# Performance work log

Measured on AMD Instinct MI355X. Metric: run time of the kernel, lower is better.

## Reference

```python
import jax, jax.numpy as jnp
import numpy as np

DIM = 1024
NUM_EXPERTS = 8
ACTIVE_EXPERTS = 2
EXPERT_DIM = 2048


def setup_inputs() -> dict:
    key = jax.random.key(0)
    k1, k2, k3, k4 = jax.random.split(key, 4)
    x = jax.random.normal(k1, (1, 2048, DIM), dtype=jnp.float32)
    gate_w = jax.random.normal(k2, (NUM_EXPERTS, DIM), dtype=jnp.float32) * 0.02
    balance_bias = jnp.zeros((NUM_EXPERTS,), dtype=jnp.float32)
    w1 = jax.random.normal(k3, (NUM_EXPERTS, EXPERT_DIM, DIM), dtype=jnp.float32) * 0.02
    w2 = jax.random.normal(k4, (NUM_EXPERTS, DIM, EXPERT_DIM), dtype=jnp.float32) * 0.02
    return {"x": x, "gate_w": gate_w, "balance_bias": balance_bias, "w1": w1, "w2": w2}


def reference(x, gate_w, balance_bias, w1, w2):
    B, S, D = x.shape
    T = B * S
    xf = x.reshape(T, D)
    # gating: sigmoid scores with load-balance bias, then top-k
    gate_logits = jnp.einsum('td,ed->te', xf, gate_w)
    gate_scores = jax.nn.sigmoid(gate_logits + balance_bias)
    topk_scores, topk_idx = jax.lax.top_k(gate_scores, ACTIVE_EXPERTS)
    topk_scores = topk_scores / (topk_scores.sum(axis=-1, keepdims=True) + 1e-6)
    # scatter normalized scores into dense combine weights [T, E]
    comb = jnp.zeros((T, NUM_EXPERTS), dtype=x.dtype)
    comb = comb.at[jnp.arange(T)[:, None], topk_idx].add(topk_scores)
    # expert FFNs (dense over experts; combine weight zeroes unselected)
    h = jax.nn.silu(jnp.einsum('td,ehd->teh', xf, w1))   # [T, E, expert_dim]
    expert_out = jnp.einsum('teh,edh->ted', h, w2)        # [T, E, D]
    out = jnp.einsum('te,ted->td', comb, expert_out)
    return out.reshape(B, S, D)
```

## Files before the change

kernel.cpp:

```cpp
#include <hip/hip_runtime.h>

#define T 2048
#define DIM 1024
#define NE 8
#define ED 2048
#define NSLOT (T * 2)
#define KSPLIT 2

#define BM 128
#define BN 64
#define BK 32
#define MAXWL 40

typedef __attribute__((ext_vector_type(8))) short s8v;
typedef __attribute__((ext_vector_type(4))) float f32x4;

__device__ __forceinline__ short f2bf(float f) {
    union { float f; unsigned u; } v;
    v.f = f;
    unsigned r = 0x7FFFu + ((v.u >> 16) & 1u);
    v.u += r;
    return (short)(v.u >> 16);
}

__device__ __forceinline__ float bf2f(short s) {
    union { unsigned u; float f; } v;
    v.u = ((unsigned)(unsigned short)s) << 16;
    return v.f;
}

__device__ __forceinline__ unsigned pkbf2(float lo, float hi) {
    union { float f; unsigned u; } a, b;
    a.f = lo; b.f = hi;
    return __builtin_amdgcn_perm(b.u + 0x8000u, a.u + 0x8000u, 0x07060302u);
}

__device__ __forceinline__ void glds16(const void* g, void* l) {
    __builtin_amdgcn_global_load_lds(
        (const __attribute__((address_space(1))) void*)g,
        (__attribute__((address_space(3))) void*)l, 16, 0, 0);
}

__global__ __launch_bounds__(256) void convert_kernel(const float* __restrict__ src,
                                                      short* __restrict__ dst, int n8) {
    int stride = gridDim.x * 256;
    for (int i = blockIdx.x * 256 + threadIdx.x; i < n8; i += stride) {
        float4 a = ((const float4*)src)[2 * i];
        float4 b = ((const float4*)src)[2 * i + 1];
        uint4 o = { pkbf2(a.x, a.y), pkbf2(a.z, a.w), pkbf2(b.x, b.y), pkbf2(b.z, b.w) };
        ((uint4*)dst)[i] = o;
    }
}

__global__ void router_kernel(const float* __restrict__ x,
                              const float* __restrict__ gw,
                              const float* __restrict__ bias,
                              short* __restrict__ xb,
                              int* __restrict__ counts,
                              int* __restrict__ top2i,
                              float* __restrict__ top2w) {
    int wid = threadIdx.x >> 6;
    int lane = threadIdx.x & 63;
    int t = blockIdx.x * 4 + wid;

    const float* xr = x + (size_t)t * DIM + lane * 16;
    float4 xv[4];
#pragma unroll
    for (int j = 0; j < 4; ++j) xv[j] = *(const float4*)(xr + j * 4);

    s8v o0, o1;
#pragma unroll
    for (int j = 0; j < 2; ++j) {
        o0[j * 4 + 0] = f2bf(xv[j].x); o0[j * 4 + 1] = f2bf(xv[j].y);
        o0[j * 4 + 2] = f2bf(xv[j].z); o0[j * 4 + 3] = f2bf(xv[j].w);
        o1[j * 4 + 0] = f2bf(xv[j + 2].x); o1[j * 4 + 1] = f2bf(xv[j + 2].y);
        o1[j * 4 + 2] = f2bf(xv[j + 2].z); o1[j * 4 + 3] = f2bf(xv[j + 2].w);
    }
    *(s8v*)(xb + (size_t)t * DIM + lane * 16) = o0;
    *(s8v*)(xb + (size_t)t * DIM + lane * 16 + 8) = o1;

    float sc[NE];
#pragma unroll
    for (int e = 0; e < NE; ++e) {
        const float* gr = gw + e * DIM + lane * 16;
        float p = 0.f;
#pragma unroll
        for (int j = 0; j < 4; ++j) {
            float4 g = *(const float4*)(gr + j * 4);
            p += xv[j].x * g.x + xv[j].y * g.y + xv[j].z * g.z + xv[j].w * g.w;
        }
#pragma unroll
        for (int off = 32; off; off >>= 1) p += __shfl_xor(p, off, 64);
        sc[e] = 1.f / (1.f + __expf(-(p + bias[e])));
    }
    int b0 = 0; float s0 = sc[0];
#pragma unroll
    for (int e = 1; e < NE; ++e) if (sc[e] > s0) { s0 = sc[e]; b0 = e; }
    int b1 = -1; float s1 = -1e30f;
#pragma unroll
    for (int e = 0; e < NE; ++e) if (e != b0 && sc[e] > s1) { s1 = sc[e]; b1 = e; }
    float inv = 1.f / (s0 + s1 + 1e-6f);
    if (lane == 0) {
        top2i[t * 2 + 0] = b0; top2i[t * 2 + 1] = b1;
        top2w[t * 2 + 0] = s0 * inv; top2w[t * 2 + 1] = s1 * inv;
        atomicAdd(&counts[b0], 1);
        atomicAdd(&counts[b1], 1);
    }
}

__global__ __launch_bounds__(256) void plan_kernel(
    const int* __restrict__ counts, const int* __restrict__ top2i,
    int* __restrict__ offsets, int* __restrict__ tok_list, int* __restrict__ slot_of,
    int* __restrict__ wl, int* __restrict__ nwl) {
    __shared__ int soff[NE];
    __shared__ int srun[NE];
    if (threadIdx.x == 0) {
        int a = 0;
        for (int e = 0; e < NE; ++e) { soff[e] = a; offsets[e] = a; a += counts[e]; srun[e] = 0; }
        int n = 0;
        for (int e = 0; e < NE; ++e) {
            int mt = (counts[e] + BM - 1) / BM;
            for (int m = 0; m < mt; ++m) wl[n++] = (e << 16) | m;
        }
        *nwl = n;
    }
    __syncthreads();
    for (int t = threadIdx.x; t < T; t += 256) {
#pragma unroll
        for (int k = 0; k < 2; ++k) {
            int e = top2i[t * 2 + k];
            int pos = atomicAdd(&srun[e], 1);
            int slot = soff[e] + pos;
            tok_list[slot] = t;
            slot_of[t * 2 + k] = slot;
        }
    }
}

template <int BF>
__global__ __launch_bounds__(256) void ffn1_kernel(
    const short* __restrict__ xb, const float* __restrict__ w1,
    const short* __restrict__ wb,
    const int* __restrict__ counts, const int* __restrict__ offsets,
    const int* __restrict__ tok_list, const int* __restrict__ wl,
    const int* __restrict__ nwl, short* __restrict__ h) {
    int my = blockIdx.y;
    if (my >= *nwl) return;
    int e = wl[my] >> 16;
    int m0 = (wl[my] & 0xffff) * BM;
    int cnt = counts[e];
    int off = offsets[e];
    int n0 = blockIdx.x * BN;

    __shared__ __align__(16) short As[2][4][BM][8];
    __shared__ __align__(16) short Bs[2][4][BN][8];

    int tid = threadIdx.x;
    int lane = tid & 63, w = tid >> 6;
    int mo = w * 32;
    int lrow = lane & 15, lq = lane >> 4;

    f32x4 acc[2][4];
#pragma unroll
    for (int mi = 0; mi < 2; ++mi)
#pragma unroll
        for (int ni = 0; ni < 4; ++ni) acc[mi][ni] = (f32x4){0.f, 0.f, 0.f, 0.f};

    int ra0 = m0 + lane;      if (ra0 > cnt - 1) ra0 = cnt - 1;
    int ra1 = m0 + 64 + lane; if (ra1 > cnt - 1) ra1 = cnt - 1;
    const short* a0 = xb + (size_t)tok_list[off + ra0] * DIM + w * 8;
    const short* a1 = xb + (size_t)tok_list[off + ra1] * DIM + w * 8;

    const short* b0 = wb + ((size_t)e * ED + n0 + lane) * DIM + w * 8;
    int br = tid >> 2, bq = tid & 3;
    const float* bp = w1 + ((size_t)e * ED + n0 + br) * DIM + bq * 8;

    const int NK = DIM / BK;

    if constexpr (BF) {
        auto stage = [&](int s, int b) {
            int k0 = s * BK;
            glds16(a0 + k0, &As[b][w][0][0]);
            glds16(a1 + k0, &As[b][w][64][0]);
            glds16(b0 + k0, &Bs[b][w][0][0]);
        };
        stage(0, 0);
        for (int kk = 0; kk < NK; ++kk) {
            int cur = kk & 1, nxt = cur ^ 1;
            __syncthreads();
            if (kk + 1 < NK) stage(kk + 1, nxt);
            s8v af[2], bfr[4];
#pragma unroll
            for (int mi = 0; mi < 2; ++mi) af[mi] = *(const s8v*)&As[cur][lq][mo + mi * 16 + lrow][0];
#pragma unroll
            for (int ni = 0; ni < 4; ++ni) bfr[ni] = *(const s8v*)&Bs[cur][lq][ni * 16 + lrow][0];
#pragma unroll
            for (int mi = 0; mi < 2; ++mi)
#pragma unroll
                for (int ni = 0; ni < 4; ++ni)
                    acc[mi][ni] = __builtin_amdgcn_mfma_f32_16x16x32_bf16(af[mi], bfr[ni], acc[mi][ni], 0, 0, 0);
        }
    } else {
        float4 L0, L1;
        glds16(a0, &As[0][w][0][0]);
        glds16(a1, &As[0][w][64][0]);
        L0 = *(const float4*)(bp); L1 = *(const float4*)(bp + 4);
        {
            uint4 p0 = { pkbf2(L0.x, L0.y), pkbf2(L0.z, L0.w), pkbf2(L1.x, L1.y), pkbf2(L1.z, L1.w) };
            *(uint4*)&Bs[0][bq][br][0] = p0;
        }
        L0 = *(const float4*)(bp + BK); L1 = *(const float4*)(bp + BK + 4);
        for (int kk = 0; kk < NK; ++kk) {
            int cur = kk & 1, nxt = cur ^ 1;
            __syncthreads();
            if (kk + 1 < NK) {
                int k0 = (kk + 1) * BK;
                glds16(a0 + k0, &As[nxt][w][0][0]);
                glds16(a1 + k0, &As[nxt][w][64][0]);
                uint4 p0 = { pkbf2(L0.x, L0.y), pkbf2(L0.z, L0.w), pkbf2(L1.x, L1.y), pkbf2(L1.z, L1.w) };
                *(uint4*)&Bs[nxt][bq][br][0] = p0;
                if (kk + 2 < NK) {
                    const float* bpp = bp + (kk + 2) * BK;
                    L0 = *(const float4*)(bpp); L1 = *(const float4*)(bpp + 4);
                }
            }
            s8v af[2], bfr[4];
#pragma unroll
            for (int mi = 0; mi < 2; ++mi) af[mi] = *(const s8v*)&As[cur][lq][mo + mi * 16 + lrow][0];
#pragma unroll
            for (int ni = 0; ni < 4; ++ni) bfr[ni] = *(const s8v*)&Bs[cur][lq][ni * 16 + lrow][0];
#pragma unroll
            for (int mi = 0; mi < 2; ++mi)
#pragma unroll
                for (int ni = 0; ni < 4; ++ni)
                    acc[mi][ni] = __builtin_amdgcn_mfma_f32_16x16x32_bf16(af[mi], bfr[ni], acc[mi][ni], 0, 0, 0);
        }
    }

#pragma unroll
    for (int mi = 0; mi < 2; ++mi) {
#pragma unroll
        for (int ni = 0; ni < 4; ++ni) {
            int ln = n0 + ni * 16 + lrow;
#pragma unroll
            for (int r = 0; r < 4; ++r) {
                int row = m0 + mo + mi * 16 + lq * 4 + r;
                if (row < cnt) {
                    float v = acc[mi][ni][r];
                    v = v / (1.f + __expf(-v));
                    h[(size_t)(off + row) * ED + ln] = f2bf(v);
                }
            }
        }
    }
}

template <int BF>
__global__ __launch_bounds__(256) void ffn2_kernel(
    const short* __restrict__ h, const float* __restrict__ w2,
    const short* __restrict__ wb,
    const int* __restrict__ counts, const int* __restrict__ offsets,
    const int* __restrict__ wl, const int* __restrict__ nwl,
    short* __restrict__ eo) {
    int my = blockIdx.y;
    if (my >= *nwl) return;
    int e = wl[my] >> 16;
    int m0 = (wl[my] & 0xffff) * BM;
    int ksp = blockIdx.z;
    int cnt = counts[e];
    int off = offsets[e];
    int n0 = blockIdx.x * BN;
    const int kbase = ksp * (ED / KSPLIT);

    __shared__ __align__(16) short As[2][4][BM][8];
    __shared__ __align__(16) short Bs[2][4][BN][8];

    int tid = threadIdx.x;
    int lane = tid & 63, w = tid >> 6;
    int mo = w * 32;
    int lrow = lane & 15, lq = lane >> 4;

    f32x4 acc[2][4];
#pragma unroll
    for (int mi = 0; mi < 2; ++mi)
#pragma unroll
        for (int ni = 0; ni < 4; ++ni) acc[mi][ni] = (f32x4){0.f, 0.f, 0.f, 0.f};

    int ra0 = m0 + lane;      if (ra0 > cnt - 1) ra0 = cnt - 1;
    int ra1 = m0 + 64 + lane; if (ra1 > cnt - 1) ra1 = cnt - 1;
    const short* a0 = h + (size_t)(off + ra0) * ED + kbase + w * 8;
    const short* a1 = h + (size_t)(off + ra1) * ED + kbase + w * 8;

    const short* b0 = wb + ((size_t)e * DIM + n0 + lane) * ED + kbase + w * 8;
    int br = tid >> 2, bq = tid & 3;
    const float* bp = w2 + ((size_t)e * DIM + n0 + br) * ED + kbase + bq * 8;

    const int NK = (ED / KSPLIT) / BK;

    if constexpr (BF) {
        auto stage = [&](int s, int b) {
            int k0 = s * BK;
            glds16(a0 + k0, &As[b][w][0][0]);
            glds16(a1 + k0, &As[b][w][64][0]);
            glds16(b0 + k0, &Bs[b][w][0][0]);
        };
        stage(0, 0);
        for (int kk = 0; kk < NK; ++kk) {
            int cur = kk & 1, nxt = cur ^ 1;
            __syncthreads();
            if (kk + 1 < NK) stage(kk + 1, nxt);
            s8v af[2], bfr[4];
#pragma unroll
            for (int mi = 0; mi < 2; ++mi) af[mi] = *(const s8v*)&As[cur][lq][mo + mi * 16 + lrow][0];
#pragma unroll
            for (int ni = 0; ni < 4; ++ni) bfr[ni] = *(const s8v*)&Bs[cur][lq][ni * 16 + lrow][0];
#pragma unroll
            for (int mi = 0; mi < 2; ++mi)
#pragma unroll
                for (int ni = 0; ni < 4; ++ni)
                    acc[mi][ni] = __builtin_amdgcn_mfma_f32_16x16x32_bf16(af[mi], bfr[ni], acc[mi][ni], 0, 0, 0);
        }
    } else {
        float4 L0, L1;
        glds16(a0, &As[0][w][0][0]);
        glds16(a1, &As[0][w][64][0]);
        L0 = *(const float4*)(bp); L1 = *(const float4*)(bp + 4);
        {
            uint4 p0 = { pkbf2(L0.x, L0.y), pkbf2(L0.z, L0.w), pkbf2(L1.x, L1.y), pkbf2(L1.z, L1.w) };
            *(uint4*)&Bs[0][bq][br][0] = p0;
        }
        L0 = *(const float4*)(bp + BK); L1 = *(const float4*)(bp + BK + 4);
        for (int kk = 0; kk < NK; ++kk) {
            int cur = kk & 1, nxt = cur ^ 1;
            __syncthreads();
            if (kk + 1 < NK) {
                int k0 = (kk + 1) * BK;
                glds16(a0 + k0, &As[nxt][w][0][0]);
                glds16(a1 + k0, &As[nxt][w][64][0]);
                uint4 p0 = { pkbf2(L0.x, L0.y), pkbf2(L0.z, L0.w), pkbf2(L1.x, L1.y), pkbf2(L1.z, L1.w) };
                *(uint4*)&Bs[nxt][bq][br][0] = p0;
                if (kk + 2 < NK) {
                    const float* bpp = bp + (kk + 2) * BK;
                    L0 = *(const float4*)(bpp); L1 = *(const float4*)(bpp + 4);
                }
            }
            s8v af[2], bfr[4];
#pragma unroll
            for (int mi = 0; mi < 2; ++mi) af[mi] = *(const s8v*)&As[cur][lq][mo + mi * 16 + lrow][0];
#pragma unroll
            for (int ni = 0; ni < 4; ++ni) bfr[ni] = *(const s8v*)&Bs[cur][lq][ni * 16 + lrow][0];
#pragma unroll
            for (int mi = 0; mi < 2; ++mi)
#pragma unroll
                for (int ni = 0; ni < 4; ++ni)
                    acc[mi][ni] = __builtin_amdgcn_mfma_f32_16x16x32_bf16(af[mi], bfr[ni], acc[mi][ni], 0, 0, 0);
        }
    }

    short* eop = eo + (size_t)ksp * NSLOT * DIM;
#pragma unroll
    for (int mi = 0; mi < 2; ++mi) {
#pragma unroll
        for (int ni = 0; ni < 4; ++ni) {
            int ln = n0 + ni * 16 + lrow;
#pragma unroll
            for (int r = 0; r < 4; ++r) {
                int row = m0 + mo + mi * 16 + lq * 4 + r;
                if (row < cnt) {
                    eop[(size_t)(off + row) * DIM + ln] = f2bf(acc[mi][ni][r]);
                }
            }
        }
    }
}

__global__ __launch_bounds__(256) void combine_kernel(
    const short* __restrict__ eo, const int* __restrict__ slot_of,
    const float* __restrict__ top2w, float* __restrict__ out) {
    int idx = blockIdx.x * 256 + threadIdx.x;
    int t = idx >> 7;
    int c = idx & 127;
    int s0 = slot_of[2 * t], s1 = slot_of[2 * t + 1];
    float w0 = top2w[2 * t], w1 = top2w[2 * t + 1];
    const short* e0 = eo;
    const short* e1 = eo + (size_t)NSLOT * DIM;
    s8v a0 = *(const s8v*)(e0 + (size_t)s0 * DIM + c * 8);
    s8v a1 = *(const s8v*)(e1 + (size_t)s0 * DIM + c * 8);
    s8v b0 = *(const s8v*)(e0 + (size_t)s1 * DIM + c * 8);
    s8v b1 = *(const s8v*)(e1 + (size_t)s1 * DIM + c * 8);
    float4 o[2];
#pragma unroll
    for (int j = 0; j < 8; ++j) {
        float v = w0 * (bf2f(a0[j]) + bf2f(a1[j])) + w1 * (bf2f(b0[j]) + bf2f(b1[j]));
        ((float*)o)[j] = v;
    }
    float4* op = (float4*)(out + (size_t)t * DIM + c * 8);
    op[0] = o[0];
    op[1] = o[1];
}

extern "C" void kernel_launch(void* const* d_in, const int* in_sizes, int n_in,
                              void* d_out, int out_size, void* d_ws, size_t ws_size,
                              hipStream_t stream) {
    const float* x    = (const float*)d_in[0];
    const float* gw   = (const float*)d_in[1];
    const float* bias = (const float*)d_in[2];
    const float* w1   = (const float*)d_in[3];
    const float* w2   = (const float*)d_in[4];
    float* out = (float*)d_out;

    char* ws = (char*)d_ws;
    short* xb = (short*)ws;
    short* h  = (short*)(ws + (4ull << 20));
    short* eo = (short*)(ws + (20ull << 20));
    char* meta = ws + (36ull << 20);
    int*   counts   = (int*)(meta);
    int*   offsets  = (int*)(meta + 64);
    int*   tok_list = (int*)(meta + 128);
    int*   slot_of  = (int*)(meta + 128 + 4 * NSLOT);
    int*   top2i    = (int*)(meta + 128 + 8 * NSLOT);
    float* top2w    = (float*)(meta + 128 + 8 * NSLOT + 8 * T);
    int*   wl       = (int*)(meta + 128 + 8 * NSLOT + 16 * T);
    int*   nwl      = (int*)(meta + 128 + 8 * NSLOT + 16 * T + 4 * MAXWL);
    short* wb       = (short*)(ws + (37ull << 20));

    bool bf = ws_size >= (70ull << 20);

    hipMemsetAsync(counts, 0, 32, stream);

    if (bf) {
        convert_kernel<<<2048, 256, 0, stream>>>(w1, wb, NE * ED * DIM / 8);
    }
    router_kernel<<<T / 4, 256, 0, stream>>>(x, gw, bias, xb, counts, top2i, top2w);
    plan_kernel<<<1, 256, 0, stream>>>(counts, top2i, offsets, tok_list, slot_of, wl, nwl);
    if (bf) {
        ffn1_kernel<1><<<dim3(ED / BN, MAXWL), 256, 0, stream>>>(xb, w1, wb, counts, offsets, tok_list, wl, nwl, h);
        convert_kernel<<<2048, 256, 0, stream>>>(w2, wb, NE * DIM * ED / 8);
        ffn2_kernel<1><<<dim3(DIM / BN, MAXWL, KSPLIT), 256, 0, stream>>>(h, w2, wb, counts, offsets, wl, nwl, eo);
    } else {
        ffn1_kernel<0><<<dim3(ED / BN, MAXWL), 256, 0, stream>>>(xb, w1, nullptr, counts, offsets, tok_list, wl, nwl, h);
        ffn2_kernel<0><<<dim3(DIM / BN, MAXWL, KSPLIT), 256, 0, stream>>>(h, w2, nullptr, counts, offsets, wl, nwl, eo);
    }
    combine_kernel<<<T * DIM / 8 / 256, 256, 0, stream>>>(eo, slot_of, top2w, out);
}
```

Before: 351.7 us.

## Interleave experts across flat 1D grid instead of per-expert worklist

Drops the worklist that plan_kernel built and maps each block directly from a flat 1D grid index. The low three bits of the block index pick the expert, so consecutive blocks touch different experts' weights. Blocks beyond an expert's tile count exit early. This removes the serial worklist construction, and the interleaving is meant to spread weight traffic and balance load across CUs. The cost is a much larger grid (sized for 16 M-tiles per expert) with many blocks that launch and immediately return.

```diff
diff --git a/kernel.cpp b/kernel.cpp
--- a/kernel.cpp
+++ b/kernel.cpp
@@ -10,7 +10,6 @@
 #define BM 128
 #define BN 64
 #define BK 32
-#define MAXWL 40
 
 typedef __attribute__((ext_vector_type(8))) short s8v;
 typedef __attribute__((ext_vector_type(4))) float f32x4;
@@ -110,19 +109,12 @@
 
 __global__ __launch_bounds__(256) void plan_kernel(
     const int* __restrict__ counts, const int* __restrict__ top2i,
-    int* __restrict__ offsets, int* __restrict__ tok_list, int* __restrict__ slot_of,
-    int* __restrict__ wl, int* __restrict__ nwl) {
+    int* __restrict__ offsets, int* __restrict__ tok_list, int* __restrict__ slot_of) {
     __shared__ int soff[NE];
     __shared__ int srun[NE];
     if (threadIdx.x == 0) {
         int a = 0;
         for (int e = 0; e < NE; ++e) { soff[e] = a; offsets[e] = a; a += counts[e]; srun[e] = 0; }
-        int n = 0;
-        for (int e = 0; e < NE; ++e) {
-            int mt = (counts[e] + BM - 1) / BM;
-            for (int m = 0; m < mt; ++m) wl[n++] = (e << 16) | m;
-        }
-        *nwl = n;
     }
     __syncthreads();
     for (int t = threadIdx.x; t < T; t += 256) {
@@ -142,15 +134,16 @@
     const short* __restrict__ xb, const float* __restrict__ w1,
     const short* __restrict__ wb,
     const int* __restrict__ counts, const int* __restrict__ offsets,
-    const int* __restrict__ tok_list, const int* __restrict__ wl,
-    const int* __restrict__ nwl, short* __restrict__ h) {
-    int my = blockIdx.y;
-    if (my >= *nwl) return;
-    int e = wl[my] >> 16;
-    int m0 = (wl[my] & 0xffff) * BM;
+    const int* __restrict__ tok_list, short* __restrict__ h) {
+    int e = blockIdx.x & 7;
+    int j = blockIdx.x >> 3;
     int cnt = counts[e];
+    const int NT = ED / BN;
+    int mt = (cnt + BM - 1) / BM;
+    if (j >= mt * NT) return;
+    int m0 = (j / NT) * BM;
+    int n0 = (j % NT) * BN;
     int off = offsets[e];
-    int n0 = blockIdx.x * BN;
 
     __shared__ __align__(16) short As[2][4][BM][8];
     __shared__ __align__(16) short Bs[2][4][BN][8];
@@ -260,16 +253,17 @@
     const short* __restrict__ h, const float* __restrict__ w2,
     const short* __restrict__ wb,
     const int* __restrict__ counts, const int* __restrict__ offsets,
-    const int* __restrict__ wl, const int* __restrict__ nwl,
     short* __restrict__ eo) {
-    int my = blockIdx.y;
-    if (my >= *nwl) return;
-    int e = wl[my] >> 16;
-    int m0 = (wl[my] & 0xffff) * BM;
-    int ksp = blockIdx.z;
+    int e = blockIdx.x & 7;
+    int j = blockIdx.x >> 3;
     int cnt = counts[e];
+    const int NT = DIM / BN;
+    int mt = (cnt + BM - 1) / BM;
+    if (j >= mt * NT * KSPLIT) return;
+    int ksp = j & 1; j >>= 1;
+    int m0 = (j / NT) * BM;
+    int n0 = (j % NT) * BN;
     int off = offsets[e];
-    int n0 = blockIdx.x * BN;
     const int kbase = ksp * (ED / KSPLIT);
 
     __shared__ __align__(16) short As[2][4][BM][8];
@@ -420,26 +414,27 @@
     int*   slot_of  = (int*)(meta + 128 + 4 * NSLOT);
     int*   top2i    = (int*)(meta + 128 + 8 * NSLOT);
     float* top2w    = (float*)(meta + 128 + 8 * NSLOT + 8 * T);
-    int*   wl       = (int*)(meta + 128 + 8 * NSLOT + 16 * T);
-    int*   nwl      = (int*)(meta + 128 + 8 * NSLOT + 16 * T + 4 * MAXWL);
     short* wb       = (short*)(ws + (37ull << 20));
 
     bool bf = ws_size >= (70ull << 20);
 
     hipMemsetAsync(counts, 0, 32, stream);
+
+    const int GRID_FFN1 = 8 * 16 * (ED / BN);
+    const int GRID_FFN2 = 8 * 16 * (DIM / BN) * KSPLIT;
 
     if (bf) {
         convert_kernel<<<2048, 256, 0, stream>>>(w1, wb, NE * ED * DIM / 8);
     }
     router_kernel<<<T / 4, 256, 0, stream>>>(x, gw, bias, xb, counts, top2i, top2w);
-    plan_kernel<<<1, 256, 0, stream>>>(counts, top2i, offsets, tok_list, slot_of, wl, nwl);
+    plan_kernel<<<1, 256, 0, stream>>>(counts, top2i, offsets, tok_list, slot_of);
     if (bf) {
-        ffn1_kernel<1><<<dim3(ED / BN, MAXWL), 256, 0, stream>>>(xb, w1, wb, counts, offsets, tok_list, wl, nwl, h);
+        ffn1_kernel<1><<<GRID_FFN1, 256, 0, stream>>>(xb, w1, wb, counts, offsets, tok_list, h);
         convert_kernel<<<2048, 256, 0, stream>>>(w2, wb, NE * DIM * ED / 8);
-        ffn2_kernel<1><<<dim3(DIM / BN, MAXWL, KSPLIT), 256, 0, stream>>>(h, w2, wb, counts, offsets, wl, nwl, eo);
+        ffn2_kernel<1><<<GRID_FFN2, 256, 0, stream>>>(h, w2, wb, counts, offsets, eo);
     } else {
-        ffn1_kernel<0><<<dim3(ED / BN, MAXWL), 256, 0, stream>>>(xb, w1, nullptr, counts, offsets, tok_list, wl, nwl, h);
-        ffn2_kernel<0><<<dim3(DIM / BN, MAXWL, KSPLIT), 256, 0, stream>>>(h, w2, nullptr, counts, offsets, wl, nwl, eo);
+        ffn1_kernel<0><<<GRID_FFN1, 256, 0, stream>>>(xb, w1, nullptr, counts, offsets, tok_list, h);
+        ffn2_kernel<0><<<GRID_FFN2, 256, 0, stream>>>(h, w2, nullptr, counts, offsets, eo);
     }
     combine_kernel<<<T * DIM / 8 / 256, 256, 0, stream>>>(eo, slot_of, top2w, out);
 }
```

After: 347.4 us. No clear change (-1.2%).
